# Performance work log

Hardware: AMD Instinct MI355X
Metric: run time of the kernel (lower is better)

The kernel has to match this reference:

```python
import jax, jax.numpy as jnp
import numpy as np

# instant-ngp HashGrid config
L, F, LOG2_T, BASE, SCALE = 16, 2, 19, 16, 1.3819
T = 1 << LOG2_T
B = 1048576
_CORNERS = np.array([[(c >> 0) & 1, (c >> 1) & 1, (c >> 2) & 1] for c in range(8)], np.int32)  # [8,3]


def hash_encode(x, grid):
    # x: [B,3] in [0,1]; grid: [L,T,F] hash tables. Trilinear interp of hashed corner features.
    corners = jnp.asarray(_CORNERS)
    outs = []
    for l in range(L):  # fixed small level loop
        res = float(np.floor(BASE * SCALE ** l))
        pos = x * res
        pos0 = jnp.floor(pos)
        w = pos - pos0                                            # [B,3] trilinear fracs
        idx = pos0.astype(jnp.uint32)[:, None, :] + corners.astype(jnp.uint32)[None]  # [B,8,3]
        h = (idx[..., 0] * jnp.uint32(1)) ^ (idx[..., 1] * jnp.uint32(2654435761)) ^ (idx[..., 2] * jnp.uint32(805459861))
        h = (h & jnp.uint32(T - 1)).astype(jnp.int32)             # [B,8]
        wc = jnp.prod(jnp.where(corners[None] == 1, w[:, None, :], 1.0 - w[:, None, :]), axis=-1)  # [B,8]
        outs.append(jnp.einsum('bcf,bc->bf', grid[l][h], wc))     # [B,F]
    return jnp.concatenate(outs, axis=-1)                         # [B, L*F]


def sh16(d):
    # Spherical harmonics degree 4 (tcnn coefficients), input in [-1,1]^3
    x, y, z = d[:, 0], d[:, 1], d[:, 2]
    x2, y2, z2 = x * x, y * y, z * z
    xy, yz, xz = x * y, y * z, x * z
    one = jnp.ones_like(x)
    return jnp.stack([
        0.28209479177387814 * one,
        -0.48860251190291987 * y,
        0.48860251190291987 * z,
        -0.48860251190291987 * x,
        1.0925484305920792 * xy,
        -1.0925484305920792 * yz,
        0.94617469575755997 * z2 - 0.31539156525251999,
        -1.0925484305920792 * xz,
        0.54627421529603959 * (x2 - y2),
        0.59004358992664352 * y * (-3.0 * x2 + y2),
        2.8906114426405538 * xy * z,
        0.45704579946446572 * y * (1.0 - 5.0 * z2),
        0.3731763325901154 * z * (5.0 * z2 - 3.0),
        0.45704579946446572 * x * (1.0 - 5.0 * z2),
        1.4453057213202769 * z * (x2 - y2),
        0.59004358992664352 * x * (-x2 + 3.0 * y2),
    ], axis=-1)


def setup_inputs() -> dict:
    key = jax.random.key(0)
    ks = jax.random.split(key, 20)
    gdim, shid, chid = 15, 64, 64
    in_color = gdim + 16 + 16  # geo_feat + SH + latent = 47

    def lin(k, o, i):
        k1, k2 = jax.random.split(k)
        bound = 1.0 / np.sqrt(i)
        return (jax.random.uniform(k1, (o, i), jnp.float32, -bound, bound),
                jax.random.uniform(k2, (o,), jnp.float32, -bound, bound))

    sw0, sb0 = lin(ks[0], shid, L * F)
    sw1, sb1 = lin(ks[1], shid, shid)
    sw2, sb2 = lin(ks[2], 1 + gdim, shid)
    cw0, cb0 = lin(ks[3], chid, in_color)
    cw1, cb1 = lin(ks[4], chid, chid)
    cw2, cb2 = lin(ks[5], chid, chid)
    cw3, cb3 = lin(ks[6], 3, chid)
    return {
        'x': jax.random.uniform(ks[7], (B, 3), jnp.float32),
        'd': jax.random.normal(ks[8], (B, 3), jnp.float32),
        'n': jax.random.randint(ks[9], (B,), 0, 100, jnp.int32),
        'grid': jax.random.uniform(ks[10], (L, T, F), jnp.float32, -1e-4, 1e-4),
        'latent_emb': jax.random.normal(ks[11], (100, 16), jnp.float32) * 0.01,
        'sw0': sw0, 'sb0': sb0, 'sw1': sw1, 'sb1': sb1, 'sw2': sw2, 'sb2': sb2,
        'cw0': cw0, 'cb0': cb0, 'cw1': cw1, 'cb1': cb1, 'cw2': cw2, 'cb2': cb2, 'cw3': cw3, 'cb3': cb3,
    }


def reference(x, d, n, grid, latent_emb, sw0, sb0, sw1, sb1, sw2, sb2,
              cw0, cb0, cw1, cb1, cw2, cb2, cw3, cb3):
    h = hash_encode(x, grid)                         # [B, 32]
    h = jax.nn.relu(h @ sw0.T + sb0)
    h = jax.nn.relu(h @ sw1.T + sb1)
    s = h @ sw2.T + sb2                              # [B, 1+geo]
    sigma, geo = s[:, 0], s[:, 1:]
    dd = ((d + 1.0) * 0.5) * 2.0 - 1.0               # module maps d->[0,1]; tcnn SH maps back to [-1,1]
    cin = jnp.concatenate([geo, sh16(dd), latent_emb[n]], axis=-1)  # [B, 47]
    c = jax.nn.relu(cin @ cw0.T + cb0)
    c = jax.nn.relu(c @ cw1.T + cb1)
    c = jax.nn.relu(c @ cw2.T + cb2)
    color = jax.nn.sigmoid(c @ cw3.T + cb3)          # [B, 3]
    return sigma, color
```

## Files before the change

kernel.cpp:

```cpp
#include <hip/hip_runtime.h>
#include <hip/hip_bf16.h>
#include <hip/hip_fp8.h>


#define TBL   524288
#define TMASK (TBL - 1)
#define MPB   512
#define NTHR  1024

#define FP8_SCALE     1048576.0f
#define FP8_INV_SCALE 9.5367431640625e-7f

typedef __bf16 bf16x8 __attribute__((ext_vector_type(8)));
typedef float  f32x4  __attribute__((ext_vector_type(4)));

__device__ const float RES_TAB[16] = {
    16.f, 22.f, 30.f, 42.f, 58.f, 80.f, 111.f, 153.f,
    212.f, 294.f, 406.f, 561.f, 775.f, 1072.f, 1481.f, 2047.f
};

__device__ __forceinline__ unsigned short f2bf(float f) {
    __hip_bfloat16 h = __float2bfloat16(f);
    unsigned short u;
    __builtin_memcpy(&u, &h, 2);
    return u;
}
__device__ __forceinline__ unsigned pack2(float a, float b) {
    return (unsigned)f2bf(a) | ((unsigned)f2bf(b) << 16);
}

__device__ __forceinline__ float fp8_dec(unsigned b) {
#if defined(__has_builtin) && __has_builtin(__builtin_amdgcn_cvt_f32_fp8)
    return __builtin_amdgcn_cvt_f32_fp8((int)b, 0);
#else
    const unsigned e = (b >> 3) & 0xF, m = b & 7;
    float v = e ? ldexpf((float)(8 + m), (int)e - 10) : ldexpf((float)m, -9);
    return (b & 0x80) ? -v : v;
#endif
}
__device__ __forceinline__ unsigned short fp8_pair(float a, float b) {
#if defined(__has_builtin) && __has_builtin(__builtin_amdgcn_cvt_pk_fp8_f32)
    return (unsigned short)(__builtin_amdgcn_cvt_pk_fp8_f32(a, b, 0, false) & 0xffff);
#else
    __hip_fp8_e4m3 qa(a), qb(b);
    return (unsigned short)((unsigned)qa.__x | ((unsigned)qb.__x << 8));
#endif
}

__global__ void __launch_bounds__(1024) grid_to_fp8(
    const float2* __restrict__ g, unsigned short* __restrict__ o, int n)
{
    const int i = blockIdx.x * 1024 + threadIdx.x;
    if (i < n) {
        const float2 v = g[i];
        o[i] = fp8_pair(v.x * FP8_SCALE, v.y * FP8_SCALE);
    }
}

template<int KS, int NT, bool RELU>
__device__ __forceinline__ void mlp_layer(
    const unsigned short* a0, int s0,
    const unsigned short* a1, int s1,
    const unsigned short* __restrict__ W, int ws,
    const float* __restrict__ bias,
    unsigned short* outp, int os,
    int wave, int lane)
{
    const int lr = lane & 15, lg = lane >> 4;
    bf16x8 bfr[NT][KS];
#pragma unroll
    for (int nt = 0; nt < NT; ++nt)
#pragma unroll
        for (int ks = 0; ks < KS; ++ks)
            bfr[nt][ks] = *reinterpret_cast<const bf16x8*>(W + (nt * 16 + lr) * ws + ks * 32 + lg * 8);

#pragma unroll
    for (int mt = 0; mt < 2; ++mt) {
        const int R = wave * 32 + mt * 16;
        bf16x8 afr[KS];
        afr[0] = *reinterpret_cast<const bf16x8*>(a0 + (R + lr) * s0 + lg * 8);
        if constexpr (KS > 1)
            afr[1] = *reinterpret_cast<const bf16x8*>(a1 + (R + lr) * s1 + lg * 8);

        f32x4 acc[NT] = {};
#pragma unroll
        for (int nt = 0; nt < NT; ++nt)
#pragma unroll
            for (int ks = 0; ks < KS; ++ks)
                acc[nt] = __builtin_amdgcn_mfma_f32_16x16x32_bf16(afr[ks], bfr[nt][ks], acc[nt], 0, 0, 0);

#pragma unroll
        for (int nt = 0; nt < NT; ++nt) {
            const float b = bias[nt * 16 + lr];
#pragma unroll
            for (int r = 0; r < 4; ++r) {
                float v = acc[nt][r] + b;
                if (RELU) v = fmaxf(v, 0.f);
                outp[(R + lg * 4 + r) * os + nt * 16 + lr] = f2bf(v);
            }
        }
    }
}

template<int GM>
__global__ void __launch_bounds__(NTHR, 4) nerf_fused(
    const float* __restrict__ x, const float* __restrict__ dvec,
    const int*   __restrict__ nidx, const void* __restrict__ grid,
    const float* __restrict__ latent,
    const float* __restrict__ sw0, const float* __restrict__ sb0,
    const float* __restrict__ sw1, const float* __restrict__ sb1,
    const float* __restrict__ sw2, const float* __restrict__ sb2,
    const float* __restrict__ cw0, const float* __restrict__ cb0,
    const float* __restrict__ cw1, const float* __restrict__ cb1,
    const float* __restrict__ cw2, const float* __restrict__ cb2,
    const float* __restrict__ cw3, const float* __restrict__ cb3,
    float* __restrict__ out, int B)
{
    __shared__ __align__(16) unsigned short sW0[64 * 40];
    __shared__ __align__(16) unsigned short sW1[64 * 72];
    __shared__ __align__(16) unsigned short sW2[16 * 72];
    __shared__ __align__(16) unsigned short sC0[64 * 72];
    __shared__ __align__(16) unsigned short sC1[64 * 72];
    __shared__ __align__(16) unsigned short sC2[64 * 72];
    __shared__ __align__(16) unsigned short sC3[16 * 72];
    __shared__ float sB[352];
    __shared__ __align__(16) unsigned short sAct[MPB * 72];

    const int tid = threadIdx.x;

    for (int i = tid; i < 64 * 40; i += NTHR) { int n = i / 40, k = i % 40; sW0[i] = f2bf(k < 32 ? sw0[n * 32 + k] : 0.f); }
    for (int i = tid; i < 64 * 72; i += NTHR) { int n = i / 72, k = i % 72; sW1[i] = f2bf(k < 64 ? sw1[n * 64 + k] : 0.f); }
    for (int i = tid; i < 16 * 72; i += NTHR) { int n = i / 72, k = i % 72; sW2[i] = f2bf(k < 64 ? sw2[n * 64 + k] : 0.f); }
    for (int i = tid; i < 64 * 72; i += NTHR) {
        int n = i / 72, k = i % 72;
        float v = 0.f;
        if (k < 15) v = cw0[n * 47 + k];
        else if (k >= 32 && k < 64) v = cw0[n * 47 + k - 17];
        sC0[i] = f2bf(v);
    }
    for (int i = tid; i < 64 * 72; i += NTHR) { int n = i / 72, k = i % 72; sC1[i] = f2bf(k < 64 ? cw1[n * 64 + k] : 0.f); }
    for (int i = tid; i < 64 * 72; i += NTHR) { int n = i / 72, k = i % 72; sC2[i] = f2bf(k < 64 ? cw2[n * 64 + k] : 0.f); }
    for (int i = tid; i < 16 * 72; i += NTHR) { int n = i / 72, k = i % 72; sC3[i] = f2bf((n < 3 && k < 64) ? cw3[n * 64 + k] : 0.f); }
    if (tid < 64) {
        sB[tid]       = sb0[tid];
        sB[64 + tid]  = sb1[tid];
        sB[144 + tid] = cb0[tid];
        sB[208 + tid] = cb1[tid];
        sB[272 + tid] = cb2[tid];
    }
    if (tid < 16) {
        sB[128 + tid] = sb2[tid];
        sB[336 + tid] = (tid < 3) ? cb3[tid] : 0.f;
    }

    const int p  = tid & (MPB - 1);
    const int hv = tid >> 9;
    const long long P = (long long)blockIdx.x * MPB + p;

    if constexpr (GM == 1) {
        const float x0 = x[3 * P + 0], x1 = x[3 * P + 1], x2 = x[3 * P + 2];
        const unsigned short* __restrict__ tf = reinterpret_cast<const unsigned short*>(grid);
#pragma unroll 2
        for (int lp = 0; lp < 4; ++lp) {
            unsigned idx[2][8];
            float wxa[2][2], wya[2][2], wza[2][2];
#pragma unroll
            for (int s = 0; s < 2; ++s) {
                const int l = hv * 8 + lp * 2 + s;
                const float res = RES_TAB[l];
                const float px = x0 * res, py = x1 * res, pz = x2 * res;
                const float fx = floorf(px), fy = floorf(py), fz = floorf(pz);
                const float wx = px - fx, wy = py - fy, wz = pz - fz;
                const unsigned ix = (unsigned)fx, iy = (unsigned)fy, iz = (unsigned)fz;
                const unsigned hx0 = ix, hx1 = ix + 1u;
                const unsigned hy0 = iy * 2654435761u, hy1 = (iy + 1u) * 2654435761u;
                const unsigned hz0 = iz * 805459861u,  hz1 = (iz + 1u) * 805459861u;
                const unsigned base = (unsigned)l * (unsigned)TBL;
#pragma unroll
                for (int c = 0; c < 8; ++c) {
                    const unsigned h = ((c & 1) ? hx1 : hx0) ^ (((c >> 1) & 1) ? hy1 : hy0)
                                     ^ (((c >> 2) & 1) ? hz1 : hz0);
                    idx[s][c] = base + (h & TMASK);
                }
                wxa[s][0] = 1.f - wx; wxa[s][1] = wx;
                wya[s][0] = 1.f - wy; wya[s][1] = wy;
                wza[s][0] = 1.f - wz; wza[s][1] = wz;
            }
            unsigned short u[2][8];
#pragma unroll
            for (int s = 0; s < 2; ++s)
#pragma unroll
                for (int c = 0; c < 8; ++c)
                    u[s][c] = tf[idx[s][c]];
#pragma unroll
            for (int s = 0; s < 2; ++s) {
                float f0 = 0.f, f1 = 0.f;
#pragma unroll
                for (int c = 0; c < 8; ++c) {
                    const float wc = wxa[s][c & 1] * wya[s][(c >> 1) & 1] * wza[s][(c >> 2) & 1];
                    const unsigned uu = u[s][c];
                    f0 = fmaf(fp8_dec(uu & 0xffu), wc, f0);
                    f1 = fmaf(fp8_dec((uu >> 8) & 0xffu), wc, f1);
                }
                const int l = hv * 8 + lp * 2 + s;
                *reinterpret_cast<unsigned*>(&sAct[p * 72 + 2 * l]) =
                    pack2(f0 * FP8_INV_SCALE, f1 * FP8_INV_SCALE);
            }
        }
    } else {
        const float x0 = x[3 * P + 0], x1 = x[3 * P + 1], x2 = x[3 * P + 2];
        const float2* __restrict__ gtab = reinterpret_cast<const float2*>(grid);
#pragma unroll 2
        for (int ll = 0; ll < 8; ++ll) {
            const int l = hv * 8 + ll;
            const float res = RES_TAB[l];
            const float px = x0 * res, py = x1 * res, pz = x2 * res;
            const float fx = floorf(px), fy = floorf(py), fz = floorf(pz);
            const float wx = px - fx, wy = py - fy, wz = pz - fz;
            const unsigned ix = (unsigned)fx, iy = (unsigned)fy, iz = (unsigned)fz;
            const unsigned hx[2] = { ix, ix + 1u };
            const unsigned hy[2] = { iy * 2654435761u, (iy + 1u) * 2654435761u };
            const unsigned hz[2] = { iz * 805459861u, (iz + 1u) * 805459861u };
            const float2* tl = gtab + (size_t)l * TBL;
            float2 g[8];
#pragma unroll
            for (int c = 0; c < 8; ++c) {
                const unsigned h = hx[c & 1] ^ hy[(c >> 1) & 1] ^ hz[(c >> 2) & 1];
                g[c] = tl[h & TMASK];
            }
            const float wxa[2] = { 1.f - wx, wx }, wya[2] = { 1.f - wy, wy }, wza[2] = { 1.f - wz, wz };
            float f0 = 0.f, f1 = 0.f;
#pragma unroll
            for (int c = 0; c < 8; ++c) {
                const float wc = wxa[c & 1] * wya[(c >> 1) & 1] * wza[(c >> 2) & 1];
                f0 = fmaf(g[c].x, wc, f0);
                f1 = fmaf(g[c].y, wc, f1);
            }
            *reinterpret_cast<unsigned*>(&sAct[p * 72 + 2 * l]) = pack2(f0, f1);
        }
    }

    unsigned creg0, creg1, creg2, creg3, creg4, creg5, creg6, creg7;
    if (hv == 0) {
        const float X = dvec[3 * P + 0], Y = dvec[3 * P + 1], Z = dvec[3 * P + 2];
        const float x2 = X * X, y2 = Y * Y, z2 = Z * Z, xy = X * Y, yz = Y * Z, xz = X * Z;
        const float s0 = 0.28209479177387814f;
        const float s1 = -0.48860251190291987f * Y;
        const float s2 = 0.48860251190291987f * Z;
        const float s3 = -0.48860251190291987f * X;
        const float s4 = 1.0925484305920792f * xy;
        const float s5 = -1.0925484305920792f * yz;
        const float s6 = 0.94617469575756f * z2 - 0.31539156525252f;
        const float s7 = -1.0925484305920792f * xz;
        const float s8 = 0.5462742152960396f * (x2 - y2);
        const float s9 = 0.5900435899266435f * Y * (-3.f * x2 + y2);
        const float s10 = 2.890611442640554f * xy * Z;
        const float s11 = 0.4570457994644657f * Y * (1.f - 5.f * z2);
        const float s12 = 0.3731763325901154f * Z * (5.f * z2 - 3.f);
        const float s13 = 0.4570457994644657f * X * (1.f - 5.f * z2);
        const float s14 = 1.445305721320277f * Z * (x2 - y2);
        const float s15 = 0.5900435899266435f * X * (-x2 + 3.f * y2);
        creg0 = pack2(s0, s1);   creg1 = pack2(s2, s3);
        creg2 = pack2(s4, s5);   creg3 = pack2(s6, s7);
        creg4 = pack2(s8, s9);   creg5 = pack2(s10, s11);
        creg6 = pack2(s12, s13); creg7 = pack2(s14, s15);
    } else {
        const int id = nidx[P];
        const float4* lp = reinterpret_cast<const float4*>(latent + 16 * id);
        const float4 a = lp[0], b = lp[1], c = lp[2], d4 = lp[3];
        creg0 = pack2(a.x, a.y); creg1 = pack2(a.z, a.w);
        creg2 = pack2(b.x, b.y); creg3 = pack2(b.z, b.w);
        creg4 = pack2(c.x, c.y); creg5 = pack2(c.z, c.w);
        creg6 = pack2(d4.x, d4.y); creg7 = pack2(d4.z, d4.w);
    }

    __syncthreads();

    const int lane = tid & 63;
    const int wave = tid >> 6;

    mlp_layer<1, 4, true>(sAct, 72, nullptr, 0,    sW0, 40, sB + 0,  sAct, 72, wave, lane);
    mlp_layer<2, 4, true>(sAct, 72, sAct + 32, 72, sW1, 72, sB + 64, sAct, 72, wave, lane);

    {
        const int lr = lane & 15, lg = lane >> 4;
        const bf16x8 b0 = *reinterpret_cast<const bf16x8*>(sW2 + lr * 72 + lg * 8);
        const bf16x8 b1 = *reinterpret_cast<const bf16x8*>(sW2 + lr * 72 + 32 + lg * 8);
        const float bb = sB[128 + lr];
#pragma unroll
        for (int mt = 0; mt < 2; ++mt) {
            const int R = wave * 32 + mt * 16;
            const bf16x8 a0 = *reinterpret_cast<const bf16x8*>(sAct + (R + lr) * 72 + lg * 8);
            const bf16x8 a1 = *reinterpret_cast<const bf16x8*>(sAct + (R + lr) * 72 + 32 + lg * 8);
            f32x4 acc = {};
            acc = __builtin_amdgcn_mfma_f32_16x16x32_bf16(a0, b0, acc, 0, 0, 0);
            acc = __builtin_amdgcn_mfma_f32_16x16x32_bf16(a1, b1, acc, 0, 0, 0);
#pragma unroll
            for (int r = 0; r < 4; ++r) {
                const float v = acc[r] + bb;
                const int row = R + lg * 4 + r;
                if (lr == 0) {
                    out[(long long)blockIdx.x * MPB + row] = v;
                    sAct[row * 72 + 31] = 0;
                } else {
                    sAct[row * 72 + lr - 1] = f2bf(v);
                }
                sAct[row * 72 + 15 + lr] = 0;
            }
        }
    }

    __syncthreads();

    {
        unsigned* c2 = reinterpret_cast<unsigned*>(&sAct[p * 72 + 32 + hv * 16]);
        c2[0] = creg0; c2[1] = creg1; c2[2] = creg2; c2[3] = creg3;
        c2[4] = creg4; c2[5] = creg5; c2[6] = creg6; c2[7] = creg7;
    }

    __syncthreads();

    mlp_layer<2, 4, true>(sAct, 72, sAct + 32, 72, sC0, 72, sB + 144, sAct, 72, wave, lane);
    mlp_layer<2, 4, true>(sAct, 72, sAct + 32, 72, sC1, 72, sB + 208, sAct, 72, wave, lane);
    mlp_layer<2, 4, true>(sAct, 72, sAct + 32, 72, sC2, 72, sB + 272, sAct, 72, wave, lane);

    {
        const int lr = lane & 15, lg = lane >> 4;
        const bf16x8 b0 = *reinterpret_cast<const bf16x8*>(sC3 + lr * 72 + lg * 8);
        const bf16x8 b1 = *reinterpret_cast<const bf16x8*>(sC3 + lr * 72 + 32 + lg * 8);
        const float bb = sB[336 + lr];
#pragma unroll
        for (int mt = 0; mt < 2; ++mt) {
            const int R = wave * 32 + mt * 16;
            const bf16x8 a0 = *reinterpret_cast<const bf16x8*>(sAct + (R + lr) * 72 + lg * 8);
            const bf16x8 a1 = *reinterpret_cast<const bf16x8*>(sAct + (R + lr) * 72 + 32 + lg * 8);
            f32x4 acc = {};
            acc = __builtin_amdgcn_mfma_f32_16x16x32_bf16(a0, b0, acc, 0, 0, 0);
            acc = __builtin_amdgcn_mfma_f32_16x16x32_bf16(a1, b1, acc, 0, 0, 0);
            if (lr < 3) {
#pragma unroll
                for (int r = 0; r < 4; ++r) {
                    const float v = acc[r] + bb;
                    const long long row = (long long)blockIdx.x * MPB + R + lg * 4 + r;
                    out[(long long)B + row * 3 + lr] = 1.f / (1.f + __expf(-v));
                }
            }
        }
    }
}

extern "C" void kernel_launch(void* const* d_in, const int* in_sizes, int n_in,
                              void* d_out, int out_size, void* d_ws, size_t ws_size,
                              hipStream_t stream) {
    const float* x    = (const float*)d_in[0];
    const float* dv   = (const float*)d_in[1];
    const int*   n    = (const int*)d_in[2];
    const float* grid = (const float*)d_in[3];
    const float* lat  = (const float*)d_in[4];
    const float* sw0  = (const float*)d_in[5];
    const float* sb0  = (const float*)d_in[6];
    const float* sw1  = (const float*)d_in[7];
    const float* sb1  = (const float*)d_in[8];
    const float* sw2  = (const float*)d_in[9];
    const float* sb2  = (const float*)d_in[10];
    const float* cw0  = (const float*)d_in[11];
    const float* cb0  = (const float*)d_in[12];
    const float* cw1  = (const float*)d_in[13];
    const float* cb1  = (const float*)d_in[14];
    const float* cw2  = (const float*)d_in[15];
    const float* cb2  = (const float*)d_in[16];
    const float* cw3  = (const float*)d_in[17];
    const float* cb3  = (const float*)d_in[18];

    const int B = in_sizes[2];
    const int nblocks = B / MPB;

    const int nent = 16 * TBL;
    const size_t ws_need = (size_t)nent * 2;

    if (ws_size >= ws_need) {
        grid_to_fp8<<<dim3((nent + 1023) / 1024), dim3(1024), 0, stream>>>(
            reinterpret_cast<const float2*>(grid), (unsigned short*)d_ws, nent);
        nerf_fused<1><<<dim3(nblocks), dim3(NTHR), 0, stream>>>(
            x, dv, n, (const void*)d_ws, lat,
            sw0, sb0, sw1, sb1, sw2, sb2,
            cw0, cb0, cw1, cb1, cw2, cb2, cw3, cb3,
            (float*)d_out, B);
    } else {
        nerf_fused<0><<<dim3(nblocks), dim3(NTHR), 0, stream>>>(
            x, dv, n, (const void*)grid, lat,
            sw0, sb0, sw1, sb1, sw2, sb2,
            cw0, cb0, cw1, cb1, cw2, cb2, cw3, cb3,
            (float*)d_out, B);
    }
}
```

Before: 621.6 us.

## Halve points per block, split levels across four thread groups, stream small weights from global

Each block now handles 256 points instead of 512, with four 256-thread groups each encoding four hash levels instead of two groups of eight. Each wave now owns one 16-row MFMA tile instead of two. The first and final small weight matrices (sw0, sw2, cw3) are read straight from global memory into registers and no longer staged in LDS, which shrinks LDS use and setup work per block. This doubles the block count and repeats the weight staging prologue per fewer points. It also leaves half of each block's threads idle during the SH/latent packing step.

```diff
diff --git a/kernel.cpp b/kernel.cpp
--- a/kernel.cpp
+++ b/kernel.cpp
@@ -5,7 +5,7 @@
 
 #define TBL   524288
 #define TMASK (TBL - 1)
-#define MPB   512
+#define MPB   256
 #define NTHR  1024
 
 #define FP8_SCALE     1048576.0f
@@ -47,6 +47,16 @@
 #endif
 }
 
+__device__ __forceinline__ bf16x8 ldw8(const float* __restrict__ w) {
+    const float4 a = *reinterpret_cast<const float4*>(w);
+    const float4 b = *reinterpret_cast<const float4*>(w + 4);
+    unsigned short u[8] = { f2bf(a.x), f2bf(a.y), f2bf(a.z), f2bf(a.w),
+                            f2bf(b.x), f2bf(b.y), f2bf(b.z), f2bf(b.w) };
+    bf16x8 r;
+    __builtin_memcpy(&r, u, 16);
+    return r;
+}
+
 __global__ void __launch_bounds__(1024) grid_to_fp8(
     const float2* __restrict__ g, unsigned short* __restrict__ o, int n)
 {
@@ -58,15 +68,14 @@
 }
 
 template<int KS, int NT, bool RELU>
-__device__ __forceinline__ void mlp_layer(
+__device__ __forceinline__ void mlp_layer16(
     const unsigned short* a0, int s0,
     const unsigned short* a1, int s1,
     const unsigned short* __restrict__ W, int ws,
     const float* __restrict__ bias,
     unsigned short* outp, int os,
-    int wave, int lane)
+    int R, int lr, int lg)
 {
-    const int lr = lane & 15, lg = lane >> 4;
     bf16x8 bfr[NT][KS];
 #pragma unroll
     for (int nt = 0; nt < NT; ++nt)
@@ -74,30 +83,26 @@
         for (int ks = 0; ks < KS; ++ks)
             bfr[nt][ks] = *reinterpret_cast<const bf16x8*>(W + (nt * 16 + lr) * ws + ks * 32 + lg * 8);
 
-#pragma unroll
-    for (int mt = 0; mt < 2; ++mt) {
-        const int R = wave * 32 + mt * 16;
-        bf16x8 afr[KS];
-        afr[0] = *reinterpret_cast<const bf16x8*>(a0 + (R + lr) * s0 + lg * 8);
-        if constexpr (KS > 1)
-            afr[1] = *reinterpret_cast<const bf16x8*>(a1 + (R + lr) * s1 + lg * 8);
-
-        f32x4 acc[NT] = {};
-#pragma unroll
-        for (int nt = 0; nt < NT; ++nt)
-#pragma unroll
-            for (int ks = 0; ks < KS; ++ks)
-                acc[nt] = __builtin_amdgcn_mfma_f32_16x16x32_bf16(afr[ks], bfr[nt][ks], acc[nt], 0, 0, 0);
-
-#pragma unroll
-        for (int nt = 0; nt < NT; ++nt) {
-            const float b = bias[nt * 16 + lr];
-#pragma unroll
-            for (int r = 0; r < 4; ++r) {
-                float v = acc[nt][r] + b;
-                if (RELU) v = fmaxf(v, 0.f);
-                outp[(R + lg * 4 + r) * os + nt * 16 + lr] = f2bf(v);
-            }
+    bf16x8 afr[KS];
+    afr[0] = *reinterpret_cast<const bf16x8*>(a0 + (R + lr) * s0 + lg * 8);
+    if constexpr (KS > 1)
+        afr[1] = *reinterpret_cast<const bf16x8*>(a1 + (R + lr) * s1 + lg * 8);
+
+    f32x4 acc[NT] = {};
+#pragma unroll
+    for (int nt = 0; nt < NT; ++nt)
+#pragma unroll
+        for (int ks = 0; ks < KS; ++ks)
+            acc[nt] = __builtin_amdgcn_mfma_f32_16x16x32_bf16(afr[ks], bfr[nt][ks], acc[nt], 0, 0, 0);
+
+#pragma unroll
+    for (int nt = 0; nt < NT; ++nt) {
+        const float b = bias[nt * 16 + lr];
+#pragma unroll
+        for (int r = 0; r < 4; ++r) {
+            float v = acc[nt][r] + b;
+            if (RELU) v = fmaxf(v, 0.f);
+            outp[(R + lg * 4 + r) * os + nt * 16 + lr] = f2bf(v);
         }
     }
 }
@@ -116,21 +121,16 @@
     const float* __restrict__ cw3, const float* __restrict__ cb3,
     float* __restrict__ out, int B)
 {
-    __shared__ __align__(16) unsigned short sW0[64 * 40];
     __shared__ __align__(16) unsigned short sW1[64 * 72];
-    __shared__ __align__(16) unsigned short sW2[16 * 72];
     __shared__ __align__(16) unsigned short sC0[64 * 72];
     __shared__ __align__(16) unsigned short sC1[64 * 72];
     __shared__ __align__(16) unsigned short sC2[64 * 72];
-    __shared__ __align__(16) unsigned short sC3[16 * 72];
     __shared__ float sB[352];
     __shared__ __align__(16) unsigned short sAct[MPB * 72];
 
     const int tid = threadIdx.x;
 
-    for (int i = tid; i < 64 * 40; i += NTHR) { int n = i / 40, k = i % 40; sW0[i] = f2bf(k < 32 ? sw0[n * 32 + k] : 0.f); }
     for (int i = tid; i < 64 * 72; i += NTHR) { int n = i / 72, k = i % 72; sW1[i] = f2bf(k < 64 ? sw1[n * 64 + k] : 0.f); }
-    for (int i = tid; i < 16 * 72; i += NTHR) { int n = i / 72, k = i % 72; sW2[i] = f2bf(k < 64 ? sw2[n * 64 + k] : 0.f); }
     for (int i = tid; i < 64 * 72; i += NTHR) {
         int n = i / 72, k = i % 72;
         float v = 0.f;
@@ -140,7 +140,6 @@
     }
     for (int i = tid; i < 64 * 72; i += NTHR) { int n = i / 72, k = i % 72; sC1[i] = f2bf(k < 64 ? cw1[n * 64 + k] : 0.f); }
     for (int i = tid; i < 64 * 72; i += NTHR) { int n = i / 72, k = i % 72; sC2[i] = f2bf(k < 64 ? cw2[n * 64 + k] : 0.f); }
-    for (int i = tid; i < 16 * 72; i += NTHR) { int n = i / 72, k = i % 72; sC3[i] = f2bf((n < 3 && k < 64) ? cw3[n * 64 + k] : 0.f); }
     if (tid < 64) {
         sB[tid]       = sb0[tid];
         sB[64 + tid]  = sb1[tid];
@@ -154,19 +153,18 @@
     }
 
     const int p  = tid & (MPB - 1);
-    const int hv = tid >> 9;
+    const int qv = tid >> 8;
     const long long P = (long long)blockIdx.x * MPB + p;
 
-    if constexpr (GM == 1) {
+    {
         const float x0 = x[3 * P + 0], x1 = x[3 * P + 1], x2 = x[3 * P + 2];
-        const unsigned short* __restrict__ tf = reinterpret_cast<const unsigned short*>(grid);
-#pragma unroll 2
-        for (int lp = 0; lp < 4; ++lp) {
+#pragma unroll
+        for (int bb = 0; bb < 2; ++bb) {
             unsigned idx[2][8];
             float wxa[2][2], wya[2][2], wza[2][2];
 #pragma unroll
             for (int s = 0; s < 2; ++s) {
-                const int l = hv * 8 + lp * 2 + s;
+                const int l = qv + 8 * bb + 4 * s;
                 const float res = RES_TAB[l];
                 const float px = x0 * res, py = x1 * res, pz = x2 * res;
                 const float fx = floorf(px), fy = floorf(py), fz = floorf(pz);
@@ -186,62 +184,55 @@
                 wya[s][0] = 1.f - wy; wya[s][1] = wy;
                 wza[s][0] = 1.f - wz; wza[s][1] = wz;
             }
-            unsigned short u[2][8];
-#pragma unroll
-            for (int s = 0; s < 2; ++s)
-#pragma unroll
-                for (int c = 0; c < 8; ++c)
-                    u[s][c] = tf[idx[s][c]];
-#pragma unroll
-            for (int s = 0; s < 2; ++s) {
-                float f0 = 0.f, f1 = 0.f;
-#pragma unroll
-                for (int c = 0; c < 8; ++c) {
-                    const float wc = wxa[s][c & 1] * wya[s][(c >> 1) & 1] * wza[s][(c >> 2) & 1];
-                    const unsigned uu = u[s][c];
-                    f0 = fmaf(fp8_dec(uu & 0xffu), wc, f0);
-                    f1 = fmaf(fp8_dec((uu >> 8) & 0xffu), wc, f1);
+            if constexpr (GM == 1) {
+                const unsigned short* __restrict__ tf = reinterpret_cast<const unsigned short*>(grid);
+                unsigned short u[2][8];
+#pragma unroll
+                for (int s = 0; s < 2; ++s)
+#pragma unroll
+                    for (int c = 0; c < 8; ++c)
+                        u[s][c] = tf[idx[s][c]];
+#pragma unroll
+                for (int s = 0; s < 2; ++s) {
+                    float f0 = 0.f, f1 = 0.f;
+#pragma unroll
+                    for (int c = 0; c < 8; ++c) {
+                        const float wc = wxa[s][c & 1] * wya[s][(c >> 1) & 1] * wza[s][(c >> 2) & 1];
+                        const unsigned uu = u[s][c];
+                        f0 = fmaf(fp8_dec(uu & 0xffu), wc, f0);
+                        f1 = fmaf(fp8_dec((uu >> 8) & 0xffu), wc, f1);
+                    }
+                    const int l = qv + 8 * bb + 4 * s;
+                    *reinterpret_cast<unsigned*>(&sAct[p * 72 + 2 * l]) =
+                        pack2(f0 * FP8_INV_SCALE, f1 * FP8_INV_SCALE);
                 }
-                const int l = hv * 8 + lp * 2 + s;
-                *reinterpret_cast<unsigned*>(&sAct[p * 72 + 2 * l]) =
-                    pack2(f0 * FP8_INV_SCALE, f1 * FP8_INV_SCALE);
+            } else {
+                const float2* __restrict__ tf = reinterpret_cast<const float2*>(grid);
+                float2 g[2][8];
+#pragma unroll
+                for (int s = 0; s < 2; ++s)
+#pragma unroll
+                    for (int c = 0; c < 8; ++c)
+                        g[s][c] = tf[idx[s][c]];
+#pragma unroll
+                for (int s = 0; s < 2; ++s) {
+                    float f0 = 0.f, f1 = 0.f;
+#pragma unroll
+                    for (int c = 0; c < 8; ++c) {
+                        const float wc = wxa[s][c & 1] * wya[s][(c >> 1) & 1] * wza[s][(c >> 2) & 1];
+                        f0 = fmaf(g[s][c].x, wc, f0);
+                        f1 = fmaf(g[s][c].y, wc, f1);
+                    }
+                    const int l = qv + 8 * bb + 4 * s;
+                    *reinterpret_cast<unsigned*>(&sAct[p * 72 + 2 * l]) = pack2(f0, f1);
+                }
             }
         }
-    } else {
-        const float x0 = x[3 * P + 0], x1 = x[3 * P + 1], x2 = x[3 * P + 2];
-        const float2* __restrict__ gtab = reinterpret_cast<const float2*>(grid);
-#pragma unroll 2
-        for (int ll = 0; ll < 8; ++ll) {
-            const int l = hv * 8 + ll;
-            const float res = RES_TAB[l];
-            const float px = x0 * res, py = x1 * res, pz = x2 * res;
-            const float fx = floorf(px), fy = floorf(py), fz = floorf(pz);
-            const float wx = px - fx, wy = py - fy, wz = pz - fz;
-            const unsigned ix = (unsigned)fx, iy = (unsigned)fy, iz = (unsigned)fz;
-            const unsigned hx[2] = { ix, ix + 1u };
-            const unsigned hy[2] = { iy * 2654435761u, (iy + 1u) * 2654435761u };
-            const unsigned hz[2] = { iz * 805459861u, (iz + 1u) * 805459861u };
-            const float2* tl = gtab + (size_t)l * TBL;
-            float2 g[8];
-#pragma unroll
-            for (int c = 0; c < 8; ++c) {
-                const unsigned h = hx[c & 1] ^ hy[(c >> 1) & 1] ^ hz[(c >> 2) & 1];
-                g[c] = tl[h & TMASK];
-            }
-            const float wxa[2] = { 1.f - wx, wx }, wya[2] = { 1.f - wy, wy }, wza[2] = { 1.f - wz, wz };
-            float f0 = 0.f, f1 = 0.f;
-#pragma unroll
-            for (int c = 0; c < 8; ++c) {
-                const float wc = wxa[c & 1] * wya[(c >> 1) & 1] * wza[(c >> 2) & 1];
-                f0 = fmaf(g[c].x, wc, f0);
-                f1 = fmaf(g[c].y, wc, f1);
-            }
-            *reinterpret_cast<unsigned*>(&sAct[p * 72 + 2 * l]) = pack2(f0, f1);
-        }
-    }
-
-    unsigned creg0, creg1, creg2, creg3, creg4, creg5, creg6, creg7;
-    if (hv == 0) {
+    }
+
+    unsigned creg0 = 0, creg1 = 0, creg2 = 0, creg3 = 0,
+             creg4 = 0, creg5 = 0, creg6 = 0, creg7 = 0;
+    if (qv == 0) {
         const float X = dvec[3 * P + 0], Y = dvec[3 * P + 1], Z = dvec[3 * P + 2];
         const float x2 = X * X, y2 = Y * Y, z2 = Z * Z, xy = X * Y, yz = Y * Z, xz = X * Z;
         const float s0 = 0.28209479177387814f;
@@ -264,7 +255,7 @@
         creg2 = pack2(s4, s5);   creg3 = pack2(s6, s7);
         creg4 = pack2(s8, s9);   creg5 = pack2(s10, s11);
         creg6 = pack2(s12, s13); creg7 = pack2(s14, s15);
-    } else {
+    } else if (qv == 1) {
         const int id = nidx[P];
         const float4* lp = reinterpret_cast<const float4*>(latent + 16 * id);
         const float4 a = lp[0], b = lp[1], c = lp[2], d4 = lp[3];
@@ -278,72 +269,87 @@
 
     const int lane = tid & 63;
     const int wave = tid >> 6;
-
-    mlp_layer<1, 4, true>(sAct, 72, nullptr, 0,    sW0, 40, sB + 0,  sAct, 72, wave, lane);
-    mlp_layer<2, 4, true>(sAct, 72, sAct + 32, 72, sW1, 72, sB + 64, sAct, 72, wave, lane);
+    const int R    = wave * 16;
+    const int lr   = lane & 15, lg = lane >> 4;
 
     {
-        const int lr = lane & 15, lg = lane >> 4;
-        const bf16x8 b0 = *reinterpret_cast<const bf16x8*>(sW2 + lr * 72 + lg * 8);
-        const bf16x8 b1 = *reinterpret_cast<const bf16x8*>(sW2 + lr * 72 + 32 + lg * 8);
+        bf16x8 b[4];
+#pragma unroll
+        for (int nt = 0; nt < 4; ++nt)
+            b[nt] = ldw8(sw0 + (nt * 16 + lr) * 32 + lg * 8);
+        const bf16x8 a0 = *reinterpret_cast<const bf16x8*>(sAct + (R + lr) * 72 + lg * 8);
+        f32x4 acc[4] = {};
+#pragma unroll
+        for (int nt = 0; nt < 4; ++nt)
+            acc[nt] = __builtin_amdgcn_mfma_f32_16x16x32_bf16(a0, b[nt], acc[nt], 0, 0, 0);
+#pragma unroll
+        for (int nt = 0; nt < 4; ++nt) {
+            const float bb = sB[nt * 16 + lr];
+#pragma unroll
+            for (int r = 0; r < 4; ++r) {
+                const float v = fmaxf(acc[nt][r] + bb, 0.f);
+                sAct[(R + lg * 4 + r) * 72 + nt * 16 + lr] = f2bf(v);
+            }
+        }
+    }
+
+    mlp_layer16<2, 4, true>(sAct, 72, sAct + 32, 72, sW1, 72, sB + 64, sAct, 72, R, lr, lg);
+
+    {
+        const bf16x8 b0 = ldw8(sw2 + lr * 64 + lg * 8);
+        const bf16x8 b1 = ldw8(sw2 + lr * 64 + 32 + lg * 8);
         const float bb = sB[128 + lr];
-#pragma unroll
-        for (int mt = 0; mt < 2; ++mt) {
-            const int R = wave * 32 + mt * 16;
-            const bf16x8 a0 = *reinterpret_cast<const bf16x8*>(sAct + (R + lr) * 72 + lg * 8);
-            const bf16x8 a1 = *reinterpret_cast<const bf16x8*>(sAct + (R + lr) * 72 + 32 + lg * 8);
-            f32x4 acc = {};
-            acc = __builtin_amdgcn_mfma_f32_16x16x32_bf16(a0, b0, acc, 0, 0, 0);
-            acc = __builtin_amdgcn_mfma_f32_16x16x32_bf16(a1, b1, acc, 0, 0, 0);
+        const bf16x8 a0 = *reinterpret_cast<const bf16x8*>(sAct + (R + lr) * 72 + lg * 8);
+        const bf16x8 a1 = *reinterpret_cast<const bf16x8*>(sAct + (R + lr) * 72 + 32 + lg * 8);
+        f32x4 acc = {};
+        acc = __builtin_amdgcn_mfma_f32_16x16x32_bf16(a0, b0, acc, 0, 0, 0);
+        acc = __builtin_amdgcn_mfma_f32_16x16x32_bf16(a1, b1, acc, 0, 0, 0);
+#pragma unroll
+        for (int r = 0; r < 4; ++r) {
+            const float v = acc[r] + bb;
+            const int row = R + lg * 4 + r;
+            if (lr == 0) {
+                out[(long long)blockIdx.x * MPB + row] = v;
+                sAct[row * 72 + 31] = 0;
+            } else {
+                sAct[row * 72 + lr - 1] = f2bf(v);
+            }
+            sAct[row * 72 + 15 + lr] = 0;
+        }
+    }
+
+    __syncthreads();
+
+    if (qv < 2) {
+        unsigned* c2 = reinterpret_cast<unsigned*>(&sAct[p * 72 + 32 + qv * 16]);
+        c2[0] = creg0; c2[1] = creg1; c2[2] = creg2; c2[3] = creg3;
+        c2[4] = creg4; c2[5] = creg5; c2[6] = creg6; c2[7] = creg7;
+    }
+
+    __syncthreads();
+
+    mlp_layer16<2, 4, true>(sAct, 72, sAct + 32, 72, sC0, 72, sB + 144, sAct, 72, R, lr, lg);
+    mlp_layer16<2, 4, true>(sAct, 72, sAct + 32, 72, sC1, 72, sB + 208, sAct, 72, R, lr, lg);
+    mlp_layer16<2, 4, true>(sAct, 72, sAct + 32, 72, sC2, 72, sB + 272, sAct, 72, R, lr, lg);
+
+    {
+        bf16x8 b0 = {}, b1 = {};
+        if (lr < 3) {
+            b0 = ldw8(cw3 + lr * 64 + lg * 8);
+            b1 = ldw8(cw3 + lr * 64 + 32 + lg * 8);
+        }
+        const float bb = sB[336 + lr];
+        const bf16x8 a0 = *reinterpret_cast<const bf16x8*>(sAct + (R + lr) * 72 + lg * 8);
+        const bf16x8 a1 = *reinterpret_cast<const bf16x8*>(sAct + (R + lr) * 72 + 32 + lg * 8);
+        f32x4 acc = {};
+        acc = __builtin_amdgcn_mfma_f32_16x16x32_bf16(a0, b0, acc, 0, 0, 0);
+        acc = __builtin_amdgcn_mfma_f32_16x16x32_bf16(a1, b1, acc, 0, 0, 0);
+        if (lr < 3) {
 #pragma unroll
             for (int r = 0; r < 4; ++r) {
                 const float v = acc[r] + bb;
-                const int row = R + lg * 4 + r;
-                if (lr == 0) {
-                    out[(long long)blockIdx.x * MPB + row] = v;
-                    sAct[row * 72 + 31] = 0;
-                } else {
-                    sAct[row * 72 + lr - 1] = f2bf(v);
-                }
-                sAct[row * 72 + 15 + lr] = 0;
-            }
-        }
-    }
-
-    __syncthreads();
-
-    {
-        unsigned* c2 = reinterpret_cast<unsigned*>(&sAct[p * 72 + 32 + hv * 16]);
-        c2[0] = creg0; c2[1] = creg1; c2[2] = creg2; c2[3] = creg3;
-        c2[4] = creg4; c2[5] = creg5; c2[6] = creg6; c2[7] = creg7;
-    }
-
-    __syncthreads();
-
-    mlp_layer<2, 4, true>(sAct, 72, sAct + 32, 72, sC0, 72, sB + 144, sAct, 72, wave, lane);
-    mlp_layer<2, 4, true>(sAct, 72, sAct + 32, 72, sC1, 72, sB + 208, sAct, 72, wave, lane);
-    mlp_layer<2, 4, true>(sAct, 72, sAct + 32, 72, sC2, 72, sB + 272, sAct, 72, wave, lane);
-
-    {
-        const int lr = lane & 15, lg = lane >> 4;
-        const bf16x8 b0 = *reinterpret_cast<const bf16x8*>(sC3 + lr * 72 + lg * 8);
-        const bf16x8 b1 = *reinterpret_cast<const bf16x8*>(sC3 + lr * 72 + 32 + lg * 8);
-        const float bb = sB[336 + lr];
-#pragma unroll
-        for (int mt = 0; mt < 2; ++mt) {
-            const int R = wave * 32 + mt * 16;
-            const bf16x8 a0 = *reinterpret_cast<const bf16x8*>(sAct + (R + lr) * 72 + lg * 8);
-            const bf16x8 a1 = *reinterpret_cast<const bf16x8*>(sAct + (R + lr) * 72 + 32 + lg * 8);
-            f32x4 acc = {};
-            acc = __builtin_amdgcn_mfma_f32_16x16x32_bf16(a0, b0, acc, 0, 0, 0);
-            acc = __builtin_amdgcn_mfma_f32_16x16x32_bf16(a1, b1, acc, 0, 0, 0);
-            if (lr < 3) {
-#pragma unroll
-                for (int r = 0; r < 4; ++r) {
-                    const float v = acc[r] + bb;
-                    const long long row = (long long)blockIdx.x * MPB + R + lg * 4 + r;
-                    out[(long long)B + row * 3 + lr] = 1.f / (1.f + __expf(-v));
-                }
+                const long long row = (long long)blockIdx.x * MPB + R + lg * 4 + r;
+                out[(long long)B + row * 3 + lr] = 1.f / (1.f + __expf(-v));
             }
         }
     }
```

After: 698.0 us. +12.3%, slower.
